# Performance work log

Measured on AMD Instinct MI355X. Metric: run time of the kernel, lower is better.

Reference implementation:

```python
import jax, jax.numpy as jnp
import numpy as np

N = 50000
E = 800000
IN_DIM, HID_DIM, LAT_DIM, OUT_DIM = 128, 128, 64, 128
NEG_SLOPE = 0.2  # PyG GATConv default


def setup_inputs() -> dict:
    key = jax.random.key(0)
    ks = jax.random.split(key, 24)
    def glorot(k, shape):
        lim = float(np.sqrt(6.0 / (shape[0] + shape[-1])))
        return jax.random.uniform(k, shape, jnp.float32, -lim, lim)
    inp = {
        "x": jax.random.normal(ks[0], (N, IN_DIM), jnp.float32),
        "edge_index": jax.random.randint(ks[1], (2, E), 0, N, jnp.int32),
        "eps": jax.random.normal(ks[2], (N, LAT_DIM), jnp.float32),
        # GATConv 1 (heads=1)
        "W1": glorot(ks[3], (IN_DIM, HID_DIM)),
        "a_src1": glorot(ks[4], (HID_DIM,)),
        "a_dst1": glorot(ks[5], (HID_DIM,)),
        "b1": jnp.zeros((HID_DIM,), jnp.float32),
        # GATConv 2
        "W2": glorot(ks[6], (HID_DIM, LAT_DIM)),
        "a_src2": glorot(ks[7], (LAT_DIM,)),
        "a_dst2": glorot(ks[8], (LAT_DIM,)),
        "b2": jnp.zeros((LAT_DIM,), jnp.float32),
        # VAE heads
        "W_mu": glorot(ks[9], (LAT_DIM, LAT_DIM)),
        "b_mu": jnp.zeros((LAT_DIM,), jnp.float32),
        "W_lv": glorot(ks[10], (LAT_DIM, LAT_DIM)),
        "b_lv": jnp.zeros((LAT_DIM,), jnp.float32),
        "W_d1": glorot(ks[11], (LAT_DIM, HID_DIM)),
        "b_d1": jnp.zeros((HID_DIM,), jnp.float32),
        "W_d2": glorot(ks[12], (HID_DIM, OUT_DIM)),
        "b_d2": jnp.zeros((OUT_DIM,), jnp.float32),
    }
    return inp


def gat_conv(x, W, a_src, a_dst, b, src, dst):
    # x: [N, F_in] -> h: [N, F_out]
    h = x @ W
    # per-node attention halves (single head)
    alpha_s = h @ a_src           # [N]
    alpha_d = h @ a_dst           # [N]
    # per-edge score: leaky_relu(a_src . h_j + a_dst . h_i), edge j->i
    e = jax.nn.leaky_relu(alpha_s[src] + alpha_d[dst], NEG_SLOPE)  # [E']
    # scatter-softmax over incoming edges of each destination node
    m = jax.ops.segment_max(e, dst, num_segments=N)                # [N]
    ex = jnp.exp(e - m[dst])
    denom = jax.ops.segment_sum(ex, dst, num_segments=N)           # [N]
    w = ex / denom[dst]                                            # [E']
    # scatter-add weighted messages
    out = jax.ops.segment_sum(h[src] * w[:, None], dst, num_segments=N)
    return out + b


def reference(x, edge_index, eps, W1, a_src1, a_dst1, b1, W2, a_src2, a_dst2, b2,
              W_mu, b_mu, W_lv, b_lv, W_d1, b_d1, W_d2, b_d2):
    # add self loops (PyG GATConv default add_self_loops=True)
    loops = jnp.arange(N, dtype=edge_index.dtype)
    src = jnp.concatenate([edge_index[0], loops])
    dst = jnp.concatenate([edge_index[1], loops])

    h = jax.nn.relu(gat_conv(x, W1, a_src1, a_dst1, b1, src, dst))
    h = jax.nn.relu(gat_conv(h, W2, a_src2, a_dst2, b2, src, dst))
    mu = h @ W_mu + b_mu
    logvar = h @ W_lv + b_lv
    z = mu + eps * jnp.exp(0.5 * logvar)
    d = jax.nn.relu(z @ W_d1 + b_d1)
    recon_x = jax.nn.sigmoid(d @ W_d2 + b_d2)
    return recon_x, mu, logvar
```

## Files before the change

kernel.cpp:

```cpp
#include <hip/hip_runtime.h>
#include <stdint.h>

typedef unsigned int u32;

__device__ __forceinline__ float lrelu(float x){ return x > 0.f ? x : 0.2f*x; }

__global__ void k_hist(const int* __restrict__ dst, int* __restrict__ deg, int E){
  int e = blockIdx.x*blockDim.x + threadIdx.x;
  if (e < E) atomicAdd(&deg[dst[e]], 1);
}

__global__ void k_scan1(const int* __restrict__ deg, int* __restrict__ offs,
                        int* __restrict__ bsum, int n){
  __shared__ int lds[256];
  int t = threadIdx.x;
  int base = blockIdx.x*1024 + t*4;
  int v0 = (base+0<n)?deg[base+0]:0;
  int v1 = (base+1<n)?deg[base+1]:0;
  int v2 = (base+2<n)?deg[base+2]:0;
  int v3 = (base+3<n)?deg[base+3]:0;
  int s = v0+v1+v2+v3;
  lds[t] = s; __syncthreads();
  for (int off=1; off<256; off<<=1){
    int tmp = (t>=off)? lds[t-off] : 0;
    __syncthreads();
    lds[t] += tmp;
    __syncthreads();
  }
  int excl = lds[t] - s;
  if (t==255) bsum[blockIdx.x] = lds[255];
  if (base+0<n) offs[base+0] = excl;
  if (base+1<n) offs[base+1] = excl+v0;
  if (base+2<n) offs[base+2] = excl+v0+v1;
  if (base+3<n) offs[base+3] = excl+v0+v1+v2;
}

__global__ void k_scan2(int* bsum, int nb){
  int lane = threadIdx.x;
  int v = (lane<nb)? bsum[lane] : 0;
  int orig = v;
  for (int off=1; off<64; off<<=1){
    int t = __shfl_up(v, off);
    if (lane >= off) v += t;
  }
  if (lane<nb) bsum[lane] = v - orig;
}

__global__ void k_scan3(int* __restrict__ offs, int* __restrict__ cur,
                        const int* __restrict__ bsum, int n){
  int i = blockIdx.x*blockDim.x + threadIdx.x;
  if (i<n){ int v = offs[i] + bsum[i>>10]; offs[i]=v; cur[i]=v; }
}

__global__ void k_scatter(const int* __restrict__ src, const int* __restrict__ dst,
                          int* __restrict__ cur, int* __restrict__ adj, int E){
  int e = blockIdx.x*blockDim.x + threadIdx.x;
  if (e<E){
    int d = dst[e];
    int p = atomicAdd(&cur[d], 1);
    adj[p] = src[e];
  }
}

template<int FOUT, int RPT>
__global__ __launch_bounds__(256) void k_gemm2(const float* __restrict__ X,
    const float* __restrict__ W, const float* __restrict__ Avs,
    const float* __restrict__ Avd, float* __restrict__ H,
    float* __restrict__ AS, float* __restrict__ AD, int N){
  constexpr int CG = FOUT/4;
  constexpr int RG = 256/CG;
  constexpr int TR = RG*RPT;
  __shared__ float xs[TR*128];
  int t = threadIdx.x;
  long i0 = (long)blockIdx.x * TR;
  #pragma unroll
  for (int j=0;j<TR*128/4/256;j++){
    int idx = t + 256*j;
    int row = idx >> 5, c4 = idx & 31;
    float4 v = make_float4(0.f,0.f,0.f,0.f);
    if (i0 + row < N) v = *(const float4*)&X[(i0+row)*128 + c4*4];
    *(float4*)&xs[row*128 + c4*4] = v;
  }
  __syncthreads();
  int ci = t & (CG-1), rg = t / CG;
  const float* Wc = W + ci*4;
  float4 acc[RPT];
  #pragma unroll
  for (int r=0;r<RPT;r++) acc[r] = make_float4(0.f,0.f,0.f,0.f);
  const float* xrow = &xs[(rg*RPT)*128];
  #pragma unroll 4
  for (int k=0;k<128;k++){
    float4 w4 = *(const float4*)&Wc[k*FOUT];
    #pragma unroll
    for (int r=0;r<RPT;r++){
      float xv = xrow[r*128 + k];
      acc[r].x = fmaf(xv, w4.x, acc[r].x);
      acc[r].y = fmaf(xv, w4.y, acc[r].y);
      acc[r].z = fmaf(xv, w4.z, acc[r].z);
      acc[r].w = fmaf(xv, w4.w, acc[r].w);
    }
  }
  float4 vs = *(const float4*)&Avs[ci*4];
  float4 vd = *(const float4*)&Avd[ci*4];
  float asv[RPT], adv[RPT];
  #pragma unroll
  for (int r=0;r<RPT;r++){
    asv[r] = acc[r].x*vs.x + acc[r].y*vs.y + acc[r].z*vs.z + acc[r].w*vs.w;
    adv[r] = acc[r].x*vd.x + acc[r].y*vd.y + acc[r].z*vd.z + acc[r].w*vd.w;
  }
  #pragma unroll
  for (int off=1; off<CG; off<<=1){
    #pragma unroll
    for (int r=0;r<RPT;r++){
      asv[r] += __shfl_xor(asv[r], off);
      adv[r] += __shfl_xor(adv[r], off);
    }
  }
  long rb = i0 + rg*RPT;
  #pragma unroll
  for (int r=0;r<RPT;r++)
    if (rb + r < N) *(float4*)&H[(rb+r)*FOUT + ci*4] = acc[r];
  if (ci == 0){
    #pragma unroll
    for (int r=0;r<RPT;r++)
      if (rb + r < N){ AS[rb+r] = asv[r]; AD[rb+r] = adv[r]; }
  }
}

template<int F>
__global__ __launch_bounds__(256) void k_agg2(const float* __restrict__ H,
    const float* __restrict__ AS, const float* __restrict__ AD,
    const float* __restrict__ B, const int* __restrict__ offs,
    const int* __restrict__ deg, const int* __restrict__ adj,
    float* __restrict__ OUT, int N){
  constexpr int PL = F/4;
  constexpr int PARTS = 64/PL;
  int lane = threadIdx.x & 63;
  int i = blockIdx.x*4 + (threadIdx.x >> 6);
  if (i >= N) return;
  int start = offs[i], dg = deg[i];
  float ad = AD[i];
  float lr_self = lrelu(AS[i] + ad);
  int part = lane / PL, lp = lane % PL;
  float M, invD, wfast = 0.f;
  int sfast = i;
  if (dg <= 64){
    float lr = -1e30f;
    if (lane < dg){ sfast = adj[start+lane]; lr = lrelu(AS[sfast] + ad); }
    float m = lr;
    #pragma unroll
    for (int off=32; off; off>>=1) m = fmaxf(m, __shfl_xor(m, off));
    M = fmaxf(m, lr_self);
    float p = (lane < dg) ? __expf(lr - M) : 0.f;
    float d = p;
    #pragma unroll
    for (int off=32; off; off>>=1) d += __shfl_xor(d, off);
    invD = 1.f/(d + __expf(lr_self - M));
    wfast = p * invD;
  } else {
    float m = -1e30f, dacc = 0.f;
    for (int b0=0; b0<dg; b0+=64){
      int k = b0 + lane;
      if (k < dg){
        int s = adj[start+k];
        float lr = lrelu(AS[s] + ad);
        float mn = fmaxf(m, lr);
        dacc = dacc*__expf(m-mn) + __expf(lr-mn);
        m = mn;
      }
    }
    #pragma unroll
    for (int off=32; off; off>>=1){
      float m2 = __shfl_xor(m, off);
      float d2 = __shfl_xor(dacc, off);
      float mn = fmaxf(m, m2);
      dacc = dacc*__expf(m-mn) + d2*__expf(m2-mn);
      m = mn;
    }
    M = fmaxf(m, lr_self);
    invD = 1.f/(dacc*__expf(m-M) + __expf(lr_self-M));
  }
  float4 acc = make_float4(0.f,0.f,0.f,0.f);
  if (part == 0){
    float ws_ = __expf(lr_self - M)*invD;
    float4 hv = *(const float4*)&H[(long)i*F + lp*4];
    acc.x = ws_*hv.x; acc.y = ws_*hv.y; acc.z = ws_*hv.z; acc.w = ws_*hv.w;
  }
  for (int b0=0; b0<dg; b0+=64){
    int s_; float w_;
    if (dg <= 64){ s_ = sfast; w_ = wfast; }
    else {
      s_ = i; w_ = 0.f;
      int k = b0 + lane;
      if (k < dg){ s_ = adj[start+k]; w_ = __expf(lrelu(AS[s_]+ad) - M)*invD; }
    }
    int cnt = min(64, dg - b0);
    for (int kk=0; kk<cnt; kk += PARTS*4){
      #pragma unroll
      for (int j=0;j<4;j++){
        int e = kk + j*PARTS + part;
        int   s = __shfl(s_, e);
        float w = __shfl(w_, e);
        const float4 hv = *(const float4*)&H[(long)s*F + lp*4];
        acc.x = fmaf(w, hv.x, acc.x); acc.y = fmaf(w, hv.y, acc.y);
        acc.z = fmaf(w, hv.z, acc.z); acc.w = fmaf(w, hv.w, acc.w);
      }
    }
  }
  #pragma unroll
  for (int off=PL; off<64; off<<=1){
    acc.x += __shfl_xor(acc.x, off); acc.y += __shfl_xor(acc.y, off);
    acc.z += __shfl_xor(acc.z, off); acc.w += __shfl_xor(acc.w, off);
  }
  if (part == 0){
    float4 bv = *(const float4*)&B[lp*4];
    float4 o;
    o.x = fmaxf(acc.x+bv.x, 0.f); o.y = fmaxf(acc.y+bv.y, 0.f);
    o.z = fmaxf(acc.z+bv.z, 0.f); o.w = fmaxf(acc.w+bv.w, 0.f);
    *(float4*)&OUT[(long)i*F + lp*4] = o;
  }
}

__global__ __launch_bounds__(256) void k_head2(
    const float* __restrict__ H2, const float* __restrict__ EPS,
    const float* __restrict__ Wmu, const float* __restrict__ bmu,
    const float* __restrict__ Wlv, const float* __restrict__ blv,
    const float* __restrict__ Wd1, const float* __restrict__ bd1,
    const float* __restrict__ Wd2, const float* __restrict__ bd2,
    float* __restrict__ out_recon, float* __restrict__ out_mu,
    float* __restrict__ out_lv, int N){
  __shared__ float smem[64*128];
  float* hs  = smem;
  float* zs  = smem + 64*64;
  float* dsb = smem;
  int t = threadIdx.x;
  long i0 = (long)blockIdx.x * 64;
  #pragma unroll
  for (int j=0;j<4;j++){
    int idx = t + 256*j;
    int row = idx >> 4, c4 = idx & 15;
    float4 v = make_float4(0.f,0.f,0.f,0.f);
    if (i0 + row < N) v = *(const float4*)&H2[(i0+row)*64 + c4*4];
    *(float4*)&hs[row*64 + c4*4] = v;
  }
  __syncthreads();
  int ci = t & 31, rg = t >> 5;
  bool is_mu = (ci < 16);
  int cbase = (is_mu ? ci : ci-16)*4;
  long rb = i0 + rg*8;
  float4 acc[8];
  #pragma unroll
  for (int r=0;r<8;r++) acc[r] = make_float4(0.f,0.f,0.f,0.f);
  {
    const float* Wp = (is_mu ? Wmu : Wlv) + cbase;
    const float* xrow = &hs[(rg*8)*64];
    #pragma unroll 4
    for (int k=0;k<64;k++){
      float4 w4 = *(const float4*)&Wp[k*64];
      #pragma unroll
      for (int r=0;r<8;r++){
        float xv = xrow[r*64 + k];
        acc[r].x = fmaf(xv,w4.x,acc[r].x); acc[r].y = fmaf(xv,w4.y,acc[r].y);
        acc[r].z = fmaf(xv,w4.z,acc[r].z); acc[r].w = fmaf(xv,w4.w,acc[r].w);
      }
    }
  }
  if (!is_mu){
    float4 bv = *(const float4*)&blv[cbase];
    #pragma unroll
    for (int r=0;r<8;r++){
      float4 lv = make_float4(acc[r].x+bv.x, acc[r].y+bv.y, acc[r].z+bv.z, acc[r].w+bv.w);
      if (rb + r < N) *(float4*)&out_lv[(rb+r)*64 + cbase] = lv;
      *(float4*)&zs[(rg*8+r)*64 + cbase] = lv;
    }
  }
  __syncthreads();
  if (is_mu){
    float4 bv = *(const float4*)&bmu[cbase];
    #pragma unroll
    for (int r=0;r<8;r++){
      long i = rb + r;
      float4 mu = make_float4(acc[r].x+bv.x, acc[r].y+bv.y, acc[r].z+bv.z, acc[r].w+bv.w);
      if (i < N) *(float4*)&out_mu[i*64 + cbase] = mu;
      float4 lv = *(const float4*)&zs[(rg*8+r)*64 + cbase];
      float4 e = make_float4(0.f,0.f,0.f,0.f);
      if (i < N) e = *(const float4*)&EPS[i*64 + cbase];
      float4 z;
      z.x = fmaf(e.x, __expf(0.5f*lv.x), mu.x);
      z.y = fmaf(e.y, __expf(0.5f*lv.y), mu.y);
      z.z = fmaf(e.z, __expf(0.5f*lv.z), mu.z);
      z.w = fmaf(e.w, __expf(0.5f*lv.w), mu.w);
      *(float4*)&zs[(rg*8+r)*64 + cbase] = z;
    }
  }
  __syncthreads();
  #pragma unroll
  for (int r=0;r<8;r++) acc[r] = make_float4(0.f,0.f,0.f,0.f);
  {
    const float* Wp = Wd1 + ci*4;
    const float* xrow = &zs[(rg*8)*64];
    #pragma unroll 4
    for (int k=0;k<64;k++){
      float4 w4 = *(const float4*)&Wp[k*128];
      #pragma unroll
      for (int r=0;r<8;r++){
        float xv = xrow[r*64 + k];
        acc[r].x = fmaf(xv,w4.x,acc[r].x); acc[r].y = fmaf(xv,w4.y,acc[r].y);
        acc[r].z = fmaf(xv,w4.z,acc[r].z); acc[r].w = fmaf(xv,w4.w,acc[r].w);
      }
    }
  }
  __syncthreads();
  {
    float4 bv = *(const float4*)&bd1[ci*4];
    #pragma unroll
    for (int r=0;r<8;r++){
      float4 d;
      d.x = fmaxf(acc[r].x+bv.x, 0.f); d.y = fmaxf(acc[r].y+bv.y, 0.f);
      d.z = fmaxf(acc[r].z+bv.z, 0.f); d.w = fmaxf(acc[r].w+bv.w, 0.f);
      *(float4*)&dsb[(rg*8+r)*128 + ci*4] = d;
    }
  }
  __syncthreads();
  #pragma unroll
  for (int r=0;r<8;r++) acc[r] = make_float4(0.f,0.f,0.f,0.f);
  {
    const float* Wp = Wd2 + ci*4;
    const float* xrow = &dsb[(rg*8)*128];
    #pragma unroll 2
    for (int k=0;k<128;k++){
      float4 w4 = *(const float4*)&Wp[k*128];
      #pragma unroll
      for (int r=0;r<8;r++){
        float xv = xrow[r*128 + k];
        acc[r].x = fmaf(xv,w4.x,acc[r].x); acc[r].y = fmaf(xv,w4.y,acc[r].y);
        acc[r].z = fmaf(xv,w4.z,acc[r].z); acc[r].w = fmaf(xv,w4.w,acc[r].w);
      }
    }
  }
  {
    float4 bv = *(const float4*)&bd2[ci*4];
    #pragma unroll
    for (int r=0;r<8;r++){
      long i = rb + r;
      if (i < N){
        float4 o;
        o.x = 1.f/(1.f+__expf(-(acc[r].x+bv.x)));
        o.y = 1.f/(1.f+__expf(-(acc[r].y+bv.y)));
        o.z = 1.f/(1.f+__expf(-(acc[r].z+bv.z)));
        o.w = 1.f/(1.f+__expf(-(acc[r].w+bv.w)));
        *(float4*)&out_recon[i*128 + ci*4] = o;
      }
    }
  }
}

extern "C" void kernel_launch(void* const* d_in, const int* in_sizes, int n_in,
                              void* d_out, int out_size, void* d_ws, size_t ws_size,
                              hipStream_t stream){
  const float* x    = (const float*)d_in[0];
  const int*   ei   = (const int*)  d_in[1];
  const float* eps  = (const float*)d_in[2];
  const float* W1   = (const float*)d_in[3];
  const float* as1v = (const float*)d_in[4];
  const float* ad1v = (const float*)d_in[5];
  const float* b1   = (const float*)d_in[6];
  const float* W2   = (const float*)d_in[7];
  const float* as2v = (const float*)d_in[8];
  const float* ad2v = (const float*)d_in[9];
  const float* b2   = (const float*)d_in[10];
  const float* Wmu  = (const float*)d_in[11];
  const float* bmu  = (const float*)d_in[12];
  const float* Wlv  = (const float*)d_in[13];
  const float* blv  = (const float*)d_in[14];
  const float* Wd1  = (const float*)d_in[15];
  const float* bd1  = (const float*)d_in[16];
  const float* Wd2  = (const float*)d_in[17];
  const float* bd2  = (const float*)d_in[18];

  const int N = in_sizes[0] / 128;
  const int E = in_sizes[1] / 2;
  const int* esrc = ei;
  const int* edst = ei + E;

  char* wp = (char*)d_ws;
  auto alloc = [&](size_t bytes)->char*{
    char* p = wp; wp += (bytes + 255) & ~(size_t)255; return p;
  };
  int*   deg  = (int*)  alloc((size_t)N*4);
  int*   offs = (int*)  alloc((size_t)N*4);
  int*   cur  = (int*)  alloc((size_t)N*4);
  int*   bsum = (int*)  alloc(256*4);
  int*   adj  = (int*)  alloc((size_t)E*4);
  float* h1   = (float*)alloc((size_t)N*128*4);
  float* o1   = (float*)alloc((size_t)N*128*4);
  float* AS1  = (float*)alloc((size_t)N*4);
  float* AD1  = (float*)alloc((size_t)N*4);
  float* AS2  = (float*)alloc((size_t)N*4);
  float* AD2  = (float*)alloc((size_t)N*4);
  float* h2 = h1;
  float* o2 = h1 + (size_t)N*64;
  (void)ws_size; (void)n_in; (void)out_size;

  float* out_recon = (float*)d_out;
  float* out_mu    = out_recon + (size_t)N*128;
  float* out_lv    = out_mu    + (size_t)N*64;

  hipMemsetAsync(deg, 0, (size_t)N*4, stream);
  int eb = (E + 255)/256;
  int nb = (N + 1023)/1024;
  k_hist   <<<eb, 256, 0, stream>>>(edst, deg, E);
  k_scan1  <<<nb, 256, 0, stream>>>(deg, offs, bsum, N);
  k_scan2  <<<1,   64, 0, stream>>>(bsum, nb);
  k_scan3  <<<(N+255)/256, 256, 0, stream>>>(offs, cur, bsum, N);
  k_scatter<<<eb, 256, 0, stream>>>(esrc, edst, cur, adj, E);

  int wb = (N+3)/4;
  int gb = (N+63)/64;
  k_gemm2<128,8><<<gb, 256, 0, stream>>>(x,  W1, as1v, ad1v, h1, AS1, AD1, N);
  k_agg2<128>   <<<wb, 256, 0, stream>>>(h1, AS1, AD1, b1, offs, deg, adj, o1, N);
  k_gemm2<64,4> <<<gb, 256, 0, stream>>>(o1, W2, as2v, ad2v, h2, AS2, AD2, N);
  k_agg2<64>    <<<wb, 256, 0, stream>>>(h2, AS2, AD2, b2, offs, deg, adj, o2, N);
  k_head2       <<<gb, 256, 0, stream>>>(o2, eps, Wmu, bmu, Wlv, blv, Wd1, bd1, Wd2, bd2,
                                         out_recon, out_mu, out_lv, N);
}
```

Measured before the change: 423.4 us.

## Move GAT and VAE-head GEMMs to split-bf16 MFMA and store H in bf16

Replaces the scalar FP32 FMA GEMMs in both GAT projections and the VAE head with bf16 MFMA 16x16x32. Each FP32 operand is split into hi and lo bf16 parts and three MFMAs are issued per tile to keep near-FP32 accuracy. Weights are transposed and split once per call by a new conversion kernel, and LDS tiles use an XOR swizzle. The projected features H are stored as bf16, which halves the gather traffic in the edge aggregation kernels. The cost is reduced precision in the aggregated messages, an extra kernel launch, and several new MFMA-based kernels to maintain.

After: 420.2 us. About the same (-0.8%).

```diff
diff --git a/kernel.cpp b/kernel.cpp
--- a/kernel.cpp
+++ b/kernel.cpp
@@ -1,8 +1,21 @@
 #include <hip/hip_runtime.h>
 #include <stdint.h>
 
+typedef unsigned short u16;
 typedef unsigned int u32;
-
+typedef short bfrag __attribute__((ext_vector_type(8)));
+typedef float f32x4 __attribute__((ext_vector_type(4)));
+
+__device__ __forceinline__ u16 f2bf(float f){
+  u32 x = __float_as_uint(f);
+  return (u16)((x + 0x7FFFu + ((x >> 16) & 1u)) >> 16);
+}
+__device__ __forceinline__ float bf2f(u16 u){ return __uint_as_float(((u32)u)<<16); }
+__device__ __forceinline__ void split1(float v, u16* h, u16* l){
+  u16 hh = f2bf(v);
+  *h = hh;
+  *l = f2bf(v - bf2f(hh));
+}
 __device__ __forceinline__ float lrelu(float x){ return x > 0.f ? x : 0.2f*x; }
 
 __global__ void k_hist(const int* __restrict__ dst, int* __restrict__ deg, int E){
@@ -62,78 +75,133 @@
   }
 }
 
-template<int FOUT, int RPT>
-__global__ __launch_bounds__(256) void k_gemm2(const float* __restrict__ X,
-    const float* __restrict__ W, const float* __restrict__ Avs,
-    const float* __restrict__ Avd, float* __restrict__ H,
-    float* __restrict__ AS, float* __restrict__ AD, int N){
-  constexpr int CG = FOUT/4;
-  constexpr int RG = 256/CG;
-  constexpr int TR = RG*RPT;
-  __shared__ float xs[TR*128];
+__global__ void k_cvtw(const float* __restrict__ W1, const float* __restrict__ W2,
+                       const float* __restrict__ Wmu, const float* __restrict__ Wlv,
+                       const float* __restrict__ Wd1, const float* __restrict__ Wd2,
+                       u16* __restrict__ hi, u16* __restrict__ lo){
+  int idx = blockIdx.x*256 + threadIdx.x;
+  float v;
+  if (idx < 16384){
+    int c = idx >> 7, k = idx & 127; v = W1[k*128 + c];
+  } else if (idx < 24576){
+    int q = idx - 16384; int c = q >> 7, k = q & 127; v = W2[k*64 + c];
+  } else if (idx < 32768){
+    int q = idx - 24576; int c = q >> 6, k = q & 63;
+    v = (c < 64) ? Wmu[k*64 + c] : Wlv[k*64 + (c-64)];
+  } else if (idx < 40960){
+    int q = idx - 32768; int c = q >> 6, k = q & 63; v = Wd1[k*128 + c];
+  } else {
+    int q = idx - 40960; int c = q >> 7, k = q & 127; v = Wd2[k*128 + c];
+  }
+  u16 h, l; split1(v, &h, &l);
+  hi[idx] = h; lo[idx] = l;
+}
+
+template<int FOUT>
+__global__ __launch_bounds__(256) void k_gemm_m(const float* __restrict__ X,
+    const u16* __restrict__ Bt_hi, const u16* __restrict__ Bt_lo,
+    const float* __restrict__ Avs, const float* __restrict__ Avd,
+    u16* __restrict__ H, float* __restrict__ AS, float* __restrict__ AD, int N){
+  constexpr int CT = FOUT/16;
+  __shared__ __align__(16) u16 xs_hi[64*128];
+  __shared__ __align__(16) u16 xs_lo[64*128];
   int t = threadIdx.x;
-  long i0 = (long)blockIdx.x * TR;
-  #pragma unroll
-  for (int j=0;j<TR*128/4/256;j++){
+  long i0 = (long)blockIdx.x * 64;
+  #pragma unroll
+  for (int j=0;j<8;j++){
     int idx = t + 256*j;
     int row = idx >> 5, c4 = idx & 31;
     float4 v = make_float4(0.f,0.f,0.f,0.f);
     if (i0 + row < N) v = *(const float4*)&X[(i0+row)*128 + c4*4];
-    *(float4*)&xs[row*128 + c4*4] = v;
+    u16 h0,h1,h2,h3,l0,l1,l2,l3;
+    split1(v.x,&h0,&l0); split1(v.y,&h1,&l1); split1(v.z,&h2,&l2); split1(v.w,&h3,&l3);
+    int off = row*128 + (((c4>>1) ^ (row&7))<<3) + (c4&1)*4;
+    *(uint2*)&xs_hi[off] = make_uint2((u32)h0 | ((u32)h1<<16), (u32)h2 | ((u32)h3<<16));
+    *(uint2*)&xs_lo[off] = make_uint2((u32)l0 | ((u32)l1<<16), (u32)l2 | ((u32)l3<<16));
   }
   __syncthreads();
-  int ci = t & (CG-1), rg = t / CG;
-  const float* Wc = W + ci*4;
-  float4 acc[RPT];
-  #pragma unroll
-  for (int r=0;r<RPT;r++) acc[r] = make_float4(0.f,0.f,0.f,0.f);
-  const float* xrow = &xs[(rg*RPT)*128];
-  #pragma unroll 4
-  for (int k=0;k<128;k++){
-    float4 w4 = *(const float4*)&Wc[k*FOUT];
-    #pragma unroll
-    for (int r=0;r<RPT;r++){
-      float xv = xrow[r*128 + k];
-      acc[r].x = fmaf(xv, w4.x, acc[r].x);
-      acc[r].y = fmaf(xv, w4.y, acc[r].y);
-      acc[r].z = fmaf(xv, w4.z, acc[r].z);
-      acc[r].w = fmaf(xv, w4.w, acc[r].w);
-    }
-  }
-  float4 vs = *(const float4*)&Avs[ci*4];
-  float4 vd = *(const float4*)&Avd[ci*4];
-  float asv[RPT], adv[RPT];
-  #pragma unroll
-  for (int r=0;r<RPT;r++){
-    asv[r] = acc[r].x*vs.x + acc[r].y*vs.y + acc[r].z*vs.z + acc[r].w*vs.w;
-    adv[r] = acc[r].x*vd.x + acc[r].y*vd.y + acc[r].z*vd.z + acc[r].w*vd.w;
-  }
-  #pragma unroll
-  for (int off=1; off<CG; off<<=1){
-    #pragma unroll
-    for (int r=0;r<RPT;r++){
+  int lane = t & 63, w = t >> 6;
+  int L = lane & 15, sg = lane >> 4;
+  int rbase = w*16;
+  bfrag a_hi[4], a_lo[4];
+  #pragma unroll
+  for (int kk=0;kk<4;kk++){
+    int row = rbase + L;
+    int off = row*128 + (((kk*4+sg) ^ (row&7))<<3);
+    a_hi[kk] = *(const bfrag*)&xs_hi[off];
+    a_lo[kk] = *(const bfrag*)&xs_lo[off];
+  }
+  f32x4 acc[CT];
+  #pragma unroll
+  for (int ct=0;ct<CT;ct++){
+    acc[ct] = (f32x4){0.f,0.f,0.f,0.f};
+    int col = ct*16 + L;
+    #pragma unroll
+    for (int kk=0;kk<4;kk++){
+      int ka = kk*32 + sg*8;
+      bfrag bh = *(const bfrag*)&Bt_hi[col*128 + ka];
+      bfrag bl = *(const bfrag*)&Bt_lo[col*128 + ka];
+      acc[ct] = __builtin_amdgcn_mfma_f32_16x16x32_bf16(a_hi[kk], bh, acc[ct], 0,0,0);
+      acc[ct] = __builtin_amdgcn_mfma_f32_16x16x32_bf16(a_lo[kk], bh, acc[ct], 0,0,0);
+      acc[ct] = __builtin_amdgcn_mfma_f32_16x16x32_bf16(a_hi[kk], bl, acc[ct], 0,0,0);
+    }
+  }
+  float asv[4] = {0,0,0,0}, adv[4] = {0,0,0,0};
+  #pragma unroll
+  for (int ct=0;ct<CT;ct++){
+    int col = ct*16 + L;
+    float s = Avs[col], d_ = Avd[col];
+    #pragma unroll
+    for (int r=0;r<4;r++){
+      asv[r] = fmaf(acc[ct][r], s, asv[r]);
+      adv[r] = fmaf(acc[ct][r], d_, adv[r]);
+    }
+  }
+  #pragma unroll
+  for (int off=1; off<16; off<<=1){
+    #pragma unroll
+    for (int r=0;r<4;r++){
       asv[r] += __shfl_xor(asv[r], off);
       adv[r] += __shfl_xor(adv[r], off);
     }
   }
-  long rb = i0 + rg*RPT;
-  #pragma unroll
-  for (int r=0;r<RPT;r++)
-    if (rb + r < N) *(float4*)&H[(rb+r)*FOUT + ci*4] = acc[r];
-  if (ci == 0){
-    #pragma unroll
-    for (int r=0;r<RPT;r++)
-      if (rb + r < N){ AS[rb+r] = asv[r]; AD[rb+r] = adv[r]; }
-  }
+  #pragma unroll
+  for (int ct=0;ct<CT;ct++){
+    int col = ct*16 + L;
+    #pragma unroll
+    for (int r=0;r<4;r++){
+      long row = i0 + rbase + sg*4 + r;
+      if (row < N) H[row*FOUT + col] = f2bf(acc[ct][r]);
+    }
+  }
+  if (L == 0){
+    #pragma unroll
+    for (int r=0;r<4;r++){
+      long row = i0 + rbase + sg*4 + r;
+      if (row < N){ AS[row] = asv[r]; AD[row] = adv[r]; }
+    }
+  }
+}
+
+__device__ __forceinline__ void fma8(float w, int4 hv, float* acc){
+  u32 u0=(u32)hv.x, u1=(u32)hv.y, u2=(u32)hv.z, u3=(u32)hv.w;
+  acc[0] = fmaf(w, __uint_as_float(u0<<16), acc[0]);
+  acc[1] = fmaf(w, __uint_as_float(u0 & 0xffff0000u), acc[1]);
+  acc[2] = fmaf(w, __uint_as_float(u1<<16), acc[2]);
+  acc[3] = fmaf(w, __uint_as_float(u1 & 0xffff0000u), acc[3]);
+  acc[4] = fmaf(w, __uint_as_float(u2<<16), acc[4]);
+  acc[5] = fmaf(w, __uint_as_float(u2 & 0xffff0000u), acc[5]);
+  acc[6] = fmaf(w, __uint_as_float(u3<<16), acc[6]);
+  acc[7] = fmaf(w, __uint_as_float(u3 & 0xffff0000u), acc[7]);
 }
 
 template<int F>
-__global__ __launch_bounds__(256) void k_agg2(const float* __restrict__ H,
+__global__ __launch_bounds__(256) void k_agg2b(const u16* __restrict__ H,
     const float* __restrict__ AS, const float* __restrict__ AD,
     const float* __restrict__ B, const int* __restrict__ offs,
     const int* __restrict__ deg, const int* __restrict__ adj,
     float* __restrict__ OUT, int N){
-  constexpr int PL = F/4;
+  constexpr int PL = F/8;
   constexpr int PARTS = 64/PL;
   int lane = threadIdx.x & 63;
   int i = blockIdx.x*4 + (threadIdx.x >> 6);
@@ -180,11 +248,11 @@
     M = fmaxf(m, lr_self);
     invD = 1.f/(dacc*__expf(m-M) + __expf(lr_self-M));
   }
-  float4 acc = make_float4(0.f,0.f,0.f,0.f);
+  float acc8[8] = {0,0,0,0,0,0,0,0};
   if (part == 0){
     float ws_ = __expf(lr_self - M)*invD;
-    float4 hv = *(const float4*)&H[(long)i*F + lp*4];
-    acc.x = ws_*hv.x; acc.y = ws_*hv.y; acc.z = ws_*hv.z; acc.w = ws_*hv.w;
+    int4 hv = *(const int4*)(H + (long)i*F + lp*8);
+    fma8(ws_, hv, acc8);
   }
   for (int b0=0; b0<dg; b0+=64){
     int s_; float w_;
@@ -201,38 +269,46 @@
         int e = kk + j*PARTS + part;
         int   s = __shfl(s_, e);
         float w = __shfl(w_, e);
-        const float4 hv = *(const float4*)&H[(long)s*F + lp*4];
-        acc.x = fmaf(w, hv.x, acc.x); acc.y = fmaf(w, hv.y, acc.y);
-        acc.z = fmaf(w, hv.z, acc.z); acc.w = fmaf(w, hv.w, acc.w);
+        int4 hv = *(const int4*)(H + (long)s*F + lp*8);
+        fma8(w, hv, acc8);
       }
     }
   }
   #pragma unroll
   for (int off=PL; off<64; off<<=1){
-    acc.x += __shfl_xor(acc.x, off); acc.y += __shfl_xor(acc.y, off);
-    acc.z += __shfl_xor(acc.z, off); acc.w += __shfl_xor(acc.w, off);
+    #pragma unroll
+    for (int j=0;j<8;j++) acc8[j] += __shfl_xor(acc8[j], off);
   }
   if (part == 0){
-    float4 bv = *(const float4*)&B[lp*4];
-    float4 o;
-    o.x = fmaxf(acc.x+bv.x, 0.f); o.y = fmaxf(acc.y+bv.y, 0.f);
-    o.z = fmaxf(acc.z+bv.z, 0.f); o.w = fmaxf(acc.w+bv.w, 0.f);
-    *(float4*)&OUT[(long)i*F + lp*4] = o;
-  }
-}
-
-__global__ __launch_bounds__(256) void k_head2(
+    float4 b0v = *(const float4*)&B[lp*8];
+    float4 b1v = *(const float4*)&B[lp*8+4];
+    float4 o0, o1;
+    o0.x = fmaxf(acc8[0]+b0v.x, 0.f); o0.y = fmaxf(acc8[1]+b0v.y, 0.f);
+    o0.z = fmaxf(acc8[2]+b0v.z, 0.f); o0.w = fmaxf(acc8[3]+b0v.w, 0.f);
+    o1.x = fmaxf(acc8[4]+b1v.x, 0.f); o1.y = fmaxf(acc8[5]+b1v.y, 0.f);
+    o1.z = fmaxf(acc8[6]+b1v.z, 0.f); o1.w = fmaxf(acc8[7]+b1v.w, 0.f);
+    *(float4*)&OUT[(long)i*F + lp*8]     = o0;
+    *(float4*)&OUT[(long)i*F + lp*8 + 4] = o1;
+  }
+}
+
+__global__ __launch_bounds__(256) void k_head_m(
     const float* __restrict__ H2, const float* __restrict__ EPS,
-    const float* __restrict__ Wmu, const float* __restrict__ bmu,
-    const float* __restrict__ Wlv, const float* __restrict__ blv,
-    const float* __restrict__ Wd1, const float* __restrict__ bd1,
-    const float* __restrict__ Wd2, const float* __restrict__ bd2,
+    const u16* __restrict__ Wml_hi, const u16* __restrict__ Wml_lo,
+    const float* __restrict__ bmu, const float* __restrict__ blv,
+    const u16* __restrict__ Wd1_hi, const u16* __restrict__ Wd1_lo,
+    const float* __restrict__ bd1,
+    const u16* __restrict__ Wd2_hi, const u16* __restrict__ Wd2_lo,
+    const float* __restrict__ bd2,
     float* __restrict__ out_recon, float* __restrict__ out_mu,
     float* __restrict__ out_lv, int N){
-  __shared__ float smem[64*128];
-  float* hs  = smem;
-  float* zs  = smem + 64*64;
-  float* dsb = smem;
+  __shared__ __align__(16) u16 smem[16384];
+  u16* hs_hi = smem;
+  u16* hs_lo = smem + 4096;
+  u16* zs_hi = smem + 8192;
+  u16* zs_lo = smem + 12288;
+  u16* ds_hi = smem;
+  u16* ds_lo = smem + 8192;
   int t = threadIdx.x;
   long i0 = (long)blockIdx.x * 64;
   #pragma unroll
@@ -241,116 +317,131 @@
     int row = idx >> 4, c4 = idx & 15;
     float4 v = make_float4(0.f,0.f,0.f,0.f);
     if (i0 + row < N) v = *(const float4*)&H2[(i0+row)*64 + c4*4];
-    *(float4*)&hs[row*64 + c4*4] = v;
+    u16 h0,h1,h2,h3,l0,l1,l2,l3;
+    split1(v.x,&h0,&l0); split1(v.y,&h1,&l1); split1(v.z,&h2,&l2); split1(v.w,&h3,&l3);
+    int off = row*64 + (((c4>>1) ^ (row&7))<<3) + (c4&1)*4;
+    *(uint2*)&hs_hi[off] = make_uint2((u32)h0 | ((u32)h1<<16), (u32)h2 | ((u32)h3<<16));
+    *(uint2*)&hs_lo[off] = make_uint2((u32)l0 | ((u32)l1<<16), (u32)l2 | ((u32)l3<<16));
   }
   __syncthreads();
-  int ci = t & 31, rg = t >> 5;
-  bool is_mu = (ci < 16);
-  int cbase = (is_mu ? ci : ci-16)*4;
-  long rb = i0 + rg*8;
-  float4 acc[8];
-  #pragma unroll
-  for (int r=0;r<8;r++) acc[r] = make_float4(0.f,0.f,0.f,0.f);
+  int lane = t & 63, w = t >> 6, L = lane & 15, sg = lane >> 4;
+  int rbase = w*16;
+  f32x4 acc1[8];
   {
-    const float* Wp = (is_mu ? Wmu : Wlv) + cbase;
-    const float* xrow = &hs[(rg*8)*64];
-    #pragma unroll 4
-    for (int k=0;k<64;k++){
-      float4 w4 = *(const float4*)&Wp[k*64];
+    bfrag ah[2], al[2];
+    #pragma unroll
+    for (int kk=0;kk<2;kk++){
+      int row = rbase + L;
+      int off = row*64 + (((kk*4+sg) ^ (row&7))<<3);
+      ah[kk] = *(const bfrag*)&hs_hi[off];
+      al[kk] = *(const bfrag*)&hs_lo[off];
+    }
+    #pragma unroll
+    for (int ct=0;ct<8;ct++){
+      acc1[ct] = (f32x4){0.f,0.f,0.f,0.f};
+      int col = ct*16 + L;
       #pragma unroll
-      for (int r=0;r<8;r++){
-        float xv = xrow[r*64 + k];
-        acc[r].x = fmaf(xv,w4.x,acc[r].x); acc[r].y = fmaf(xv,w4.y,acc[r].y);
-        acc[r].z = fmaf(xv,w4.z,acc[r].z); acc[r].w = fmaf(xv,w4.w,acc[r].w);
+      for (int kk=0;kk<2;kk++){
+        int ka = kk*32 + sg*8;
+        bfrag bh = *(const bfrag*)&Wml_hi[col*64 + ka];
+        bfrag bl = *(const bfrag*)&Wml_lo[col*64 + ka];
+        acc1[ct] = __builtin_amdgcn_mfma_f32_16x16x32_bf16(ah[kk], bh, acc1[ct], 0,0,0);
+        acc1[ct] = __builtin_amdgcn_mfma_f32_16x16x32_bf16(al[kk], bh, acc1[ct], 0,0,0);
+        acc1[ct] = __builtin_amdgcn_mfma_f32_16x16x32_bf16(ah[kk], bl, acc1[ct], 0,0,0);
       }
     }
   }
-  if (!is_mu){
-    float4 bv = *(const float4*)&blv[cbase];
-    #pragma unroll
-    for (int r=0;r<8;r++){
-      float4 lv = make_float4(acc[r].x+bv.x, acc[r].y+bv.y, acc[r].z+bv.z, acc[r].w+bv.w);
-      if (rb + r < N) *(float4*)&out_lv[(rb+r)*64 + cbase] = lv;
-      *(float4*)&zs[(rg*8+r)*64 + cbase] = lv;
+  #pragma unroll
+  for (int ct=0;ct<4;ct++){
+    int c = ct*16 + L;
+    float bm = bmu[c], bl_ = blv[c];
+    #pragma unroll
+    for (int r=0;r<4;r++){
+      int row_l = rbase + sg*4 + r;
+      long i = i0 + row_l;
+      float mu = acc1[ct][r] + bm;
+      float lv = acc1[ct+4][r] + bl_;
+      float e = 0.f;
+      if (i < N){ out_mu[i*64+c] = mu; out_lv[i*64+c] = lv; e = EPS[i*64+c]; }
+      float z = fmaf(e, __expf(0.5f*lv), mu);
+      u16 zh, zl; split1(z,&zh,&zl);
+      int zo = row_l*64 + ((((c>>3)) ^ (row_l&7))<<3) + (c&7);
+      zs_hi[zo] = zh; zs_lo[zo] = zl;
+    }
+  }
+  f32x4 acc2[8];
+  {
+    bfrag ah[2], al[2];
+    #pragma unroll
+    for (int kk=0;kk<2;kk++){
+      int row = rbase + L;
+      int off = row*64 + (((kk*4+sg) ^ (row&7))<<3);
+      ah[kk] = *(const bfrag*)&zs_hi[off];
+      al[kk] = *(const bfrag*)&zs_lo[off];
+    }
+    #pragma unroll
+    for (int ct=0;ct<8;ct++){
+      acc2[ct] = (f32x4){0.f,0.f,0.f,0.f};
+      int col = ct*16 + L;
+      #pragma unroll
+      for (int kk=0;kk<2;kk++){
+        int ka = kk*32 + sg*8;
+        bfrag bh = *(const bfrag*)&Wd1_hi[col*64 + ka];
+        bfrag bl = *(const bfrag*)&Wd1_lo[col*64 + ka];
+        acc2[ct] = __builtin_amdgcn_mfma_f32_16x16x32_bf16(ah[kk], bh, acc2[ct], 0,0,0);
+        acc2[ct] = __builtin_amdgcn_mfma_f32_16x16x32_bf16(al[kk], bh, acc2[ct], 0,0,0);
+        acc2[ct] = __builtin_amdgcn_mfma_f32_16x16x32_bf16(ah[kk], bl, acc2[ct], 0,0,0);
+      }
     }
   }
   __syncthreads();
-  if (is_mu){
-    float4 bv = *(const float4*)&bmu[cbase];
-    #pragma unroll
-    for (int r=0;r<8;r++){
-      long i = rb + r;
-      float4 mu = make_float4(acc[r].x+bv.x, acc[r].y+bv.y, acc[r].z+bv.z, acc[r].w+bv.w);
-      if (i < N) *(float4*)&out_mu[i*64 + cbase] = mu;
-      float4 lv = *(const float4*)&zs[(rg*8+r)*64 + cbase];
-      float4 e = make_float4(0.f,0.f,0.f,0.f);
-      if (i < N) e = *(const float4*)&EPS[i*64 + cbase];
-      float4 z;
-      z.x = fmaf(e.x, __expf(0.5f*lv.x), mu.x);
-      z.y = fmaf(e.y, __expf(0.5f*lv.y), mu.y);
-      z.z = fmaf(e.z, __expf(0.5f*lv.z), mu.z);
-      z.w = fmaf(e.w, __expf(0.5f*lv.w), mu.w);
-      *(float4*)&zs[(rg*8+r)*64 + cbase] = z;
-    }
-  }
-  __syncthreads();
-  #pragma unroll
-  for (int r=0;r<8;r++) acc[r] = make_float4(0.f,0.f,0.f,0.f);
+  #pragma unroll
+  for (int ct=0;ct<8;ct++){
+    int c = ct*16 + L;
+    float bb = bd1[c];
+    #pragma unroll
+    for (int r=0;r<4;r++){
+      int row_l = rbase + sg*4 + r;
+      float d = fmaxf(acc2[ct][r] + bb, 0.f);
+      u16 dh, dl; split1(d,&dh,&dl);
+      int dof = row_l*128 + ((((c>>3)) ^ (row_l&7))<<3) + (c&7);
+      ds_hi[dof] = dh; ds_lo[dof] = dl;
+    }
+  }
+  f32x4 acc3[8];
   {
-    const float* Wp = Wd1 + ci*4;
-    const float* xrow = &zs[(rg*8)*64];
-    #pragma unroll 4
-    for (int k=0;k<64;k++){
-      float4 w4 = *(const float4*)&Wp[k*128];
+    bfrag ah[4], al[4];
+    #pragma unroll
+    for (int kk=0;kk<4;kk++){
+      int row = rbase + L;
+      int off = row*128 + (((kk*4+sg) ^ (row&7))<<3);
+      ah[kk] = *(const bfrag*)&ds_hi[off];
+      al[kk] = *(const bfrag*)&ds_lo[off];
+    }
+    #pragma unroll
+    for (int ct=0;ct<8;ct++){
+      acc3[ct] = (f32x4){0.f,0.f,0.f,0.f};
+      int col = ct*16 + L;
       #pragma unroll
-      for (int r=0;r<8;r++){
-        float xv = xrow[r*64 + k];
-        acc[r].x = fmaf(xv,w4.x,acc[r].x); acc[r].y = fmaf(xv,w4.y,acc[r].y);
-        acc[r].z = fmaf(xv,w4.z,acc[r].z); acc[r].w = fmaf(xv,w4.w,acc[r].w);
+      for (int kk=0;kk<4;kk++){
+        int ka = kk*32 + sg*8;
+        bfrag bh = *(const bfrag*)&Wd2_hi[col*128 + ka];
+        bfrag bl = *(const bfrag*)&Wd2_lo[col*128 + ka];
+        acc3[ct] = __builtin_amdgcn_mfma_f32_16x16x32_bf16(ah[kk], bh, acc3[ct], 0,0,0);
+        acc3[ct] = __builtin_amdgcn_mfma_f32_16x16x32_bf16(al[kk], bh, acc3[ct], 0,0,0);
+        acc3[ct] = __builtin_amdgcn_mfma_f32_16x16x32_bf16(ah[kk], bl, acc3[ct], 0,0,0);
       }
     }
   }
-  __syncthreads();
-  {
-    float4 bv = *(const float4*)&bd1[ci*4];
-    #pragma unroll
-    for (int r=0;r<8;r++){
-      float4 d;
-      d.x = fmaxf(acc[r].x+bv.x, 0.f); d.y = fmaxf(acc[r].y+bv.y, 0.f);
-      d.z = fmaxf(acc[r].z+bv.z, 0.f); d.w = fmaxf(acc[r].w+bv.w, 0.f);
-      *(float4*)&dsb[(rg*8+r)*128 + ci*4] = d;
-    }
-  }
-  __syncthreads();
-  #pragma unroll
-  for (int r=0;r<8;r++) acc[r] = make_float4(0.f,0.f,0.f,0.f);
-  {
-    const float* Wp = Wd2 + ci*4;
-    const float* xrow = &dsb[(rg*8)*128];
-    #pragma unroll 2
-    for (int k=0;k<128;k++){
-      float4 w4 = *(const float4*)&Wp[k*128];
-      #pragma unroll
-      for (int r=0;r<8;r++){
-        float xv = xrow[r*128 + k];
-        acc[r].x = fmaf(xv,w4.x,acc[r].x); acc[r].y = fmaf(xv,w4.y,acc[r].y);
-        acc[r].z = fmaf(xv,w4.z,acc[r].z); acc[r].w = fmaf(xv,w4.w,acc[r].w);
-      }
-    }
-  }
-  {
-    float4 bv = *(const float4*)&bd2[ci*4];
-    #pragma unroll
-    for (int r=0;r<8;r++){
-      long i = rb + r;
-      if (i < N){
-        float4 o;
-        o.x = 1.f/(1.f+__expf(-(acc[r].x+bv.x)));
-        o.y = 1.f/(1.f+__expf(-(acc[r].y+bv.y)));
-        o.z = 1.f/(1.f+__expf(-(acc[r].z+bv.z)));
-        o.w = 1.f/(1.f+__expf(-(acc[r].w+bv.w)));
-        *(float4*)&out_recon[i*128 + ci*4] = o;
-      }
+  #pragma unroll
+  for (int ct=0;ct<8;ct++){
+    int c = ct*16 + L;
+    float bb = bd2[c];
+    #pragma unroll
+    for (int r=0;r<4;r++){
+      long i = i0 + rbase + sg*4 + r;
+      if (i < N)
+        out_recon[i*128+c] = 1.f/(1.f+__expf(-(acc3[ct][r] + bb)));
     }
   }
 }
@@ -392,15 +483,23 @@
   int*   cur  = (int*)  alloc((size_t)N*4);
   int*   bsum = (int*)  alloc(256*4);
   int*   adj  = (int*)  alloc((size_t)E*4);
-  float* h1   = (float*)alloc((size_t)N*128*4);
+  u16*   h1b  = (u16*)  alloc((size_t)N*128*2);
   float* o1   = (float*)alloc((size_t)N*128*4);
   float* AS1  = (float*)alloc((size_t)N*4);
   float* AD1  = (float*)alloc((size_t)N*4);
   float* AS2  = (float*)alloc((size_t)N*4);
   float* AD2  = (float*)alloc((size_t)N*4);
-  float* h2 = h1;
-  float* o2 = h1 + (size_t)N*64;
+  u16*   wt_hi = (u16*) alloc(57344*2);
+  u16*   wt_lo = (u16*) alloc(57344*2);
+  u16*   h2b = h1b;
+  float* o2  = o1;
   (void)ws_size; (void)n_in; (void)out_size;
+
+  const u16 *w1t_hi = wt_hi,        *w1t_lo = wt_lo;
+  const u16 *w2t_hi = wt_hi+16384,  *w2t_lo = wt_lo+16384;
+  const u16 *wml_hi = wt_hi+24576,  *wml_lo = wt_lo+24576;
+  const u16 *wd1t_hi = wt_hi+32768, *wd1t_lo = wt_lo+32768;
+  const u16 *wd2t_hi = wt_hi+40960, *wd2t_lo = wt_lo+40960;
 
   float* out_recon = (float*)d_out;
   float* out_mu    = out_recon + (size_t)N*128;
@@ -414,13 +513,15 @@
   k_scan2  <<<1,   64, 0, stream>>>(bsum, nb);
   k_scan3  <<<(N+255)/256, 256, 0, stream>>>(offs, cur, bsum, N);
   k_scatter<<<eb, 256, 0, stream>>>(esrc, edst, cur, adj, E);
+  k_cvtw   <<<224, 256, 0, stream>>>(W1, W2, Wmu, Wlv, Wd1, Wd2, wt_hi, wt_lo);
 
   int wb = (N+3)/4;
   int gb = (N+63)/64;
-  k_gemm2<128,8><<<gb, 256, 0, stream>>>(x,  W1, as1v, ad1v, h1, AS1, AD1, N);
-  k_agg2<128>   <<<wb, 256, 0, stream>>>(h1, AS1, AD1, b1, offs, deg, adj, o1, N);
-  k_gemm2<64,4> <<<gb, 256, 0, stream>>>(o1, W2, as2v, ad2v, h2, AS2, AD2, N);
-  k_agg2<64>    <<<wb, 256, 0, stream>>>(h2, AS2, AD2, b2, offs, deg, adj, o2, N);
-  k_head2       <<<gb, 256, 0, stream>>>(o2, eps, Wmu, bmu, Wlv, blv, Wd1, bd1, Wd2, bd2,
-                                         out_recon, out_mu, out_lv, N);
-}
+  k_gemm_m<128><<<gb, 256, 0, stream>>>(x,  w1t_hi, w1t_lo, as1v, ad1v, h1b, AS1, AD1, N);
+  k_agg2b<128> <<<wb, 256, 0, stream>>>(h1b, AS1, AD1, b1, offs, deg, adj, o1, N);
+  k_gemm_m<64> <<<gb, 256, 0, stream>>>(o1, w2t_hi, w2t_lo, as2v, ad2v, h2b, AS2, AD2, N);
+  k_agg2b<64>  <<<wb, 256, 0, stream>>>(h2b, AS2, AD2, b2, offs, deg, adj, o2, N);
+  k_head_m     <<<gb, 256, 0, stream>>>(o2, eps, wml_hi, wml_lo, bmu, blv,
+                                        wd1t_hi, wd1t_lo, bd1, wd2t_hi, wd2t_lo, bd2,
+                                        out_recon, out_mu, out_lv, N);
+}
```
